# Kernel optimization log

Hardware: AMD Instinct MI355X
Metric: run time of the kernel (lower is better)

Reference implementation:

```python
import jax, jax.numpy as jnp
import numpy as np

TAU = 2.0
V_TH = 1.0
SG_ALPHA = 4.0  # spikingjelly surrogate.Sigmoid default

@jax.custom_vjp
def spike_fn(u):
    # heaviside(u) with sigmoid surrogate gradient; u = v - v_threshold
    return (u >= 0.0).astype(u.dtype)

def _spike_fwd(u):
    return spike_fn(u), u

def _spike_bwd(u, g):
    s = jax.nn.sigmoid(SG_ALPHA * u)
    return (g * SG_ALPHA * s * (1.0 - s),)

spike_fn.defvjp(_spike_fwd, _spike_bwd)

def lif_scan(h):
    # h: [T, B, D] input currents; multi-step LIF with hard reset to 0,
    # decay_input=True: v = v + (h - v) / tau
    def step(v, h_t):
        v = v + (h_t - v) / TAU
        s = spike_fn(v - V_TH)
        v = v * (1.0 - jax.lax.stop_gradient(s))  # detach_reset=True, v_reset=0
        return v, s
    v0 = jnp.zeros_like(h[0])
    _, spikes = jax.lax.scan(step, v0, h)
    return spikes  # [T, B, D]

def setup_inputs() -> dict:
    key = jax.random.key(0)
    k_x, k_w1, k_b1, k_w2, k_b2 = jax.random.split(key, 5)
    T, B, D, C = 32, 512, 1024, 1000
    lim1 = 1.0 / np.sqrt(D)
    return {
        "x": jax.random.normal(k_x, (T, B, D), dtype=jnp.float32),
        "W1": jax.random.uniform(k_w1, (D, D), jnp.float32, -lim1, lim1),
        "b1": jax.random.uniform(k_b1, (D,), jnp.float32, -lim1, lim1),
        "W2": jax.random.uniform(k_w2, (C, D), jnp.float32, -lim1, lim1),
        "b2": jax.random.uniform(k_b2, (C,), jnp.float32, -lim1, lim1),
    }

def reference(x, W1, b1, W2, b2):
    # linear_1: [T,B,D] @ [D,D]^T + b1
    h = jnp.einsum('tbd,ed->tbe', x, W1) + b1
    s = lif_scan(h)                               # [T,B,D] spikes in {0,1}
    y = jnp.einsum('tbd,cd->tbc', s, W2) + b2     # [T,B,C]
    y = y.mean(axis=0)                            # [B,C]
    return jax.nn.log_softmax(y, axis=1)
```

## Files before the change

### kernel.cpp

```cpp
#include <hip/hip_runtime.h>
#include <math.h>

#define T_STEPS 32
#define B_SZ    512
#define D_SZ    1024
#define C_SZ    1000
#define KZ      8
#define HP      132

typedef __bf16 bf16x8 __attribute__((ext_vector_type(8)));
typedef float  f32x4  __attribute__((ext_vector_type(4)));

__device__ __forceinline__ unsigned short f2bf(float f) {
    unsigned u = __float_as_uint(f);
    unsigned r = u + 0x7FFFu + ((u >> 16) & 1u);
    return (unsigned short)(r >> 16);
}
__device__ __forceinline__ float bf2f(unsigned short b) {
    return __uint_as_float(((unsigned)b) << 16);
}

__device__ __forceinline__ void async_copy16(const void* g, void* l) {
    __builtin_amdgcn_global_load_lds(
        (const __attribute__((address_space(1))) unsigned int*)g,
        (__attribute__((address_space(3))) unsigned int*)l,
        16, 0, 0);
}

__global__ __launch_bounds__(256) void cast_x_k(
    const float* __restrict__ s, unsigned short* __restrict__ d)
{
    const int idx = blockIdx.x * 256 + threadIdx.x;
    const float4 v = ((const float4*)s)[idx];
    ushort4 o;
    o.x = f2bf(v.x); o.y = f2bf(v.y); o.z = f2bf(v.z); o.w = f2bf(v.w);
    ((ushort4*)d)[idx] = o;
}

__global__ __launch_bounds__(256) void cast_w_k(
    const float* __restrict__ W1, unsigned short* __restrict__ W1o,
    const float* __restrict__ W2, unsigned short* __restrict__ W2o)
{
    const int idx = blockIdx.x * 256 + threadIdx.x;
    const int n1 = (D_SZ * D_SZ) / 4;
    const float4 v = (idx < n1) ? ((const float4*)W1)[idx]
                                : ((const float4*)W2)[idx - n1];
    ushort4 o;
    o.x = f2bf(v.x); o.y = f2bf(v.y); o.z = f2bf(v.z); o.w = f2bf(v.w);
    if (idx < n1) ((ushort4*)W1o)[idx] = o;
    else          ((ushort4*)W2o)[idx - n1] = o;
}

__global__ __launch_bounds__(256) void gemm1_scan_k(
    const unsigned short* __restrict__ A, const unsigned short* __restrict__ Bm,
    const float* __restrict__ bias, unsigned short* __restrict__ cnt)
{
    __shared__ __align__(16) unsigned short smem[128 * HP];
    unsigned short* As = smem;
    unsigned short* Bs = smem + 4096;

    const int tid  = threadIdx.x;
    const int wave = tid >> 6;
    const int lane = tid & 63;
    const int lm   = lane & 15;
    const int quad = lane >> 4;
    const int wm   = (wave >> 1) * 64;
    const int wn   = (wave & 1) * 64;

    const int f  = blockIdx.x;
    const int yb = f & 127;
    const int xb = f >> 7;
    const int b0 = yb * 4;
    const int n0 = xb * 128;

    f32x4 acc[4][4];
    #pragma unroll
    for (int i = 0; i < 4; ++i)
        #pragma unroll
        for (int j = 0; j < 4; ++j)
            acc[i][j] = (f32x4){0.f, 0.f, 0.f, 0.f};

    int srowA[2], sgq[2];
    size_t arowoff[2];
    unsigned ldsoff[2];
    #pragma unroll
    for (int p = 0; p < 2; ++p) {
        const int s = p * 256 + tid;
        const int rho = s >> 2;
        srowA[p] = rho;
        sgq[p]  = (s & 3) ^ ((rho >> 1) & 3);
        arowoff[p] = (size_t)((rho >> 2) * 512 + b0 + (rho & 3)) * D_SZ;
        ldsoff[p] = (unsigned)(p * 256 + wave * 64) * 16u;
    }
    const int fq = quad ^ ((lm >> 1) & 3);

    for (int k0 = 0; k0 < D_SZ; k0 += 32) {
        #pragma unroll
        for (int p = 0; p < 2; ++p) {
            async_copy16(A + arowoff[p] + k0 + sgq[p] * 8, (char*)As + ldsoff[p]);
            async_copy16(Bm + (size_t)(n0 + srowA[p]) * D_SZ + k0 + sgq[p] * 8,
                         (char*)Bs + ldsoff[p]);
        }
        __syncthreads();

        bf16x8 af[4], bfr[4];
        #pragma unroll
        for (int i = 0; i < 4; ++i) {
            af[i]  = ((const bf16x8*)As)[(wm + i * 16 + lm) * 4 + fq];
            bfr[i] = ((const bf16x8*)Bs)[(wn + i * 16 + lm) * 4 + fq];
        }
        #pragma unroll
        for (int mi = 0; mi < 4; ++mi)
            #pragma unroll
            for (int ni = 0; ni < 4; ++ni)
                acc[mi][ni] = __builtin_amdgcn_mfma_f32_16x16x32_bf16(
                    af[mi], bfr[ni], acc[mi][ni], 0, 0, 0);
        __syncthreads();
    }

    #pragma unroll
    for (int ni = 0; ni < 4; ++ni) {
        const int nn = wn + ni * 16 + lm;
        const float bv = bias[n0 + nn];
        #pragma unroll
        for (int mi = 0; mi < 4; ++mi) {
            const f32x4 v = acc[mi][ni];
            #pragma unroll
            for (int r = 0; r < 4; ++r)
                smem[(wm + mi * 16 + quad * 4 + r) * HP + nn] = f2bf(v[r] + bv);
        }
    }
    __syncthreads();

    #pragma unroll
    for (int rep = 0; rep < 2; ++rep) {
        const int flat = rep * 256 + tid;
        const int bb = flat >> 7;
        const int c  = flat & 127;
        float v = 0.f, cv = 0.f;
        #pragma unroll
        for (int t = 0; t < T_STEPS; ++t) {
            const float ht = bf2f(smem[(t * 4 + bb) * HP + c]);
            v = 0.5f * (v + ht);
            const float s = (v >= 1.0f) ? 1.0f : 0.0f;
            cv += s;
            v *= (1.0f - s);
        }
        cnt[(size_t)(b0 + bb) * D_SZ + n0 + c] = f2bf(cv);
    }
}

__global__ __launch_bounds__(256) void gemm2_splitk_k(
    const unsigned short* __restrict__ A, const unsigned short* __restrict__ Bm,
    float* __restrict__ partial)
{
    __shared__ __align__(16) unsigned short As[128 * 32];
    __shared__ __align__(16) unsigned short Bs[128 * 32];

    const int tid  = threadIdx.x;
    const int wave = tid >> 6;
    const int lane = tid & 63;
    const int lm   = lane & 15;
    const int quad = lane >> 4;
    const int wm   = (wave >> 1) * 64;
    const int wn   = (wave & 1) * 64;
    const int n0   = blockIdx.x * 128;
    const int m0   = blockIdx.y * 128;
    const int kz   = blockIdx.z;

    f32x4 acc[4][4];
    #pragma unroll
    for (int i = 0; i < 4; ++i)
        #pragma unroll
        for (int j = 0; j < 4; ++j)
            acc[i][j] = (f32x4){0.f, 0.f, 0.f, 0.f};

    int srow[2], sgq[2];
    unsigned ldsoff[2];
    #pragma unroll
    for (int p = 0; p < 2; ++p) {
        const int s = p * 256 + tid;
        srow[p] = s >> 2;
        sgq[p]  = (s & 3) ^ ((srow[p] >> 1) & 3);
        ldsoff[p] = (unsigned)(p * 256 + wave * 64) * 16u;
    }
    const int fq = quad ^ ((lm >> 1) & 3);

    const int kbeg = kz * (D_SZ / KZ);
    for (int k0 = kbeg; k0 < kbeg + D_SZ / KZ; k0 += 32) {
        #pragma unroll
        for (int p = 0; p < 2; ++p) {
            async_copy16(A + (size_t)(m0 + srow[p]) * D_SZ + k0 + sgq[p] * 8,
                         (char*)As + ldsoff[p]);
            int brow = n0 + srow[p];
            if (brow > C_SZ - 1) brow = C_SZ - 1;
            async_copy16(Bm + (size_t)brow * D_SZ + k0 + sgq[p] * 8,
                         (char*)Bs + ldsoff[p]);
        }
        __syncthreads();

        bf16x8 af[4], bfr[4];
        #pragma unroll
        for (int i = 0; i < 4; ++i) {
            af[i]  = ((const bf16x8*)As)[(wm + i * 16 + lm) * 4 + fq];
            bfr[i] = ((const bf16x8*)Bs)[(wn + i * 16 + lm) * 4 + fq];
        }
        #pragma unroll
        for (int mi = 0; mi < 4; ++mi)
            #pragma unroll
            for (int ni = 0; ni < 4; ++ni)
                acc[mi][ni] = __builtin_amdgcn_mfma_f32_16x16x32_bf16(
                    af[mi], bfr[ni], acc[mi][ni], 0, 0, 0);
        __syncthreads();
    }

    #pragma unroll
    for (int ni = 0; ni < 4; ++ni) {
        const int nn = n0 + wn + ni * 16 + lm;
        if (nn >= C_SZ) continue;
        #pragma unroll
        for (int mi = 0; mi < 4; ++mi) {
            const f32x4 v = acc[mi][ni];
            #pragma unroll
            for (int r = 0; r < 4; ++r) {
                const int mm = m0 + wm + mi * 16 + quad * 4 + r;
                partial[((size_t)kz * B_SZ + mm) * C_SZ + nn] = v[r];
            }
        }
    }
}

__global__ __launch_bounds__(256) void reduce_lsm_k(
    const float* __restrict__ partial, const float* __restrict__ b2,
    float* __restrict__ out)
{
    __shared__ float red_max[4];
    __shared__ float red_sum[4];

    const int b   = blockIdx.x;
    const int tid = threadIdx.x;

    float vals[4];
    float m = -1e30f;
    #pragma unroll
    for (int k = 0; k < 4; ++k) {
        const int c = tid + k * 256;
        if (c < C_SZ) {
            float s = 0.f;
            #pragma unroll
            for (int z = 0; z < KZ; ++z)
                s += partial[((size_t)z * B_SZ + b) * C_SZ + c];
            vals[k] = s * (1.0f / (float)T_STEPS) + b2[c];
        } else {
            vals[k] = -1e30f;
        }
        m = fmaxf(m, vals[k]);
    }
    #pragma unroll
    for (int off = 32; off > 0; off >>= 1)
        m = fmaxf(m, __shfl_down(m, off, 64));
    const int wave = tid >> 6;
    const int lane = tid & 63;
    if (lane == 0) red_max[wave] = m;
    __syncthreads();
    m = fmaxf(fmaxf(red_max[0], red_max[1]), fmaxf(red_max[2], red_max[3]));

    float s = 0.f;
    #pragma unroll
    for (int k = 0; k < 4; ++k) {
        const int c = tid + k * 256;
        if (c < C_SZ) s += __expf(vals[k] - m);
    }
    #pragma unroll
    for (int off = 32; off > 0; off >>= 1)
        s += __shfl_down(s, off, 64);
    if (lane == 0) red_sum[wave] = s;
    __syncthreads();
    s = red_sum[0] + red_sum[1] + red_sum[2] + red_sum[3];

    const float lse = m + logf(s);
    #pragma unroll
    for (int k = 0; k < 4; ++k) {
        const int c = tid + k * 256;
        if (c < C_SZ) out[(size_t)b * C_SZ + c] = vals[k] - lse;
    }
}

extern "C" void kernel_launch(void* const* d_in, const int* in_sizes, int n_in,
                              void* d_out, int out_size, void* d_ws, size_t ws_size,
                              hipStream_t stream)
{
    const float* x  = (const float*)d_in[0];
    const float* W1 = (const float*)d_in[1];
    const float* b1 = (const float*)d_in[2];
    const float* W2 = (const float*)d_in[3];
    const float* b2 = (const float*)d_in[4];
    float* out = (float*)d_out;

    char* ws = (char*)d_ws;
    unsigned short* x_bf    = (unsigned short*)(ws);
    unsigned short* W1_bf   = (unsigned short*)(ws + 33554432);
    unsigned short* W2_bf   = (unsigned short*)(ws + 35651584);
    unsigned short* cnt_bf  = (unsigned short*)(ws + 37699584);
    float*          partial = (float*)(ws + 38748160);

    const int MBD = T_STEPS * B_SZ;

    cast_x_k<<<(MBD * D_SZ / 4) / 256, 256, 0, stream>>>(x, x_bf);
    cast_w_k<<<((D_SZ * D_SZ + C_SZ * D_SZ) / 4) / 256, 256, 0, stream>>>(
        W1, W1_bf, W2, W2_bf);

    gemm1_scan_k<<<(B_SZ / 4) * (D_SZ / 128), 256, 0, stream>>>(
        x_bf, W1_bf, b1, cnt_bf);

    {
        dim3 grid((C_SZ + 127) / 128, B_SZ / 128, KZ);
        gemm2_splitk_k<<<grid, 256, 0, stream>>>(cnt_bf, W2_bf, partial);
    }

    reduce_lsm_k<<<B_SZ, 256, 0, stream>>>(partial, b2, out);
}
```

Before: 171.1 us.

## Fuse split-K reduction and log-softmax into GEMM2; merge cast and zeroing kernels

The two cast kernels become one that also zeroes the fp32 logits buffer and the per-row-block counters. GEMM2 now accumulates its split-K partials with float atomicAdd directly into y instead of writing a partial buffer. The last block to finish each 128-row group, found through an atomic counter, computes the mean, bias and log-softmax. This removes two launches and the partial buffer round trip. In exchange it adds atomic traffic, makes the float summation order nondeterministic, and leaves the softmax tail serialized on just four blocks.

```diff
diff --git a/kernel.cpp b/kernel.cpp
--- a/kernel.cpp
+++ b/kernel.cpp
@@ -27,28 +27,32 @@
         16, 0, 0);
 }
 
-__global__ __launch_bounds__(256) void cast_x_k(
-    const float* __restrict__ s, unsigned short* __restrict__ d)
+#define NX4  4194304
+#define NW14  262144
+#define NW24  256000
+#define NZ4   128001
+#define NTOT (NX4 + NW14 + NW24 + NZ4)
+
+__global__ __launch_bounds__(256) void cast_zero_k(
+    const float* __restrict__ x,  unsigned short* __restrict__ x_bf,
+    const float* __restrict__ W1, unsigned short* __restrict__ W1_bf,
+    const float* __restrict__ W2, unsigned short* __restrict__ W2_bf,
+    float4* __restrict__ zbase)
 {
     const int idx = blockIdx.x * 256 + threadIdx.x;
-    const float4 v = ((const float4*)s)[idx];
+    if (idx >= NTOT) return;
+    if (idx >= NX4 + NW14 + NW24) {
+        zbase[idx - (NX4 + NW14 + NW24)] = make_float4(0.f, 0.f, 0.f, 0.f);
+        return;
+    }
+    const float4* s; ushort4* d; int j;
+    if (idx < NX4)              { s = (const float4*)x;  d = (ushort4*)x_bf;  j = idx; }
+    else if (idx < NX4 + NW14)  { s = (const float4*)W1; d = (ushort4*)W1_bf; j = idx - NX4; }
+    else                        { s = (const float4*)W2; d = (ushort4*)W2_bf; j = idx - NX4 - NW14; }
+    const float4 v = s[j];
     ushort4 o;
     o.x = f2bf(v.x); o.y = f2bf(v.y); o.z = f2bf(v.z); o.w = f2bf(v.w);
-    ((ushort4*)d)[idx] = o;
-}
-
-__global__ __launch_bounds__(256) void cast_w_k(
-    const float* __restrict__ W1, unsigned short* __restrict__ W1o,
-    const float* __restrict__ W2, unsigned short* __restrict__ W2o)
-{
-    const int idx = blockIdx.x * 256 + threadIdx.x;
-    const int n1 = (D_SZ * D_SZ) / 4;
-    const float4 v = (idx < n1) ? ((const float4*)W1)[idx]
-                                : ((const float4*)W2)[idx - n1];
-    ushort4 o;
-    o.x = f2bf(v.x); o.y = f2bf(v.y); o.z = f2bf(v.z); o.w = f2bf(v.w);
-    if (idx < n1) ((ushort4*)W1o)[idx] = o;
-    else          ((ushort4*)W2o)[idx - n1] = o;
+    d[j] = o;
 }
 
 __global__ __launch_bounds__(256) void gemm1_scan_k(
@@ -150,12 +154,17 @@
     }
 }
 
-__global__ __launch_bounds__(256) void gemm2_splitk_k(
-    const unsigned short* __restrict__ A, const unsigned short* __restrict__ Bm,
-    float* __restrict__ partial)
+__global__ __launch_bounds__(256) void gemm2_lsm_k(
+    const unsigned short* __restrict__ A,
+    const unsigned short* __restrict__ Bm,
+    const float* __restrict__ b2,
+    float* __restrict__ y,
+    unsigned int* __restrict__ ctr,
+    float* __restrict__ out)
 {
     __shared__ __align__(16) unsigned short As[128 * 32];
     __shared__ __align__(16) unsigned short Bs[128 * 32];
+    __shared__ int lastFlag;
 
     const int tid  = threadIdx.x;
     const int wave = tid >> 6;
@@ -224,65 +233,63 @@
             #pragma unroll
             for (int r = 0; r < 4; ++r) {
                 const int mm = m0 + wm + mi * 16 + quad * 4 + r;
-                partial[((size_t)kz * B_SZ + mm) * C_SZ + nn] = v[r];
+                atomicAdd(&y[(size_t)mm * C_SZ + nn], v[r]);
             }
         }
     }
-}
-
-__global__ __launch_bounds__(256) void reduce_lsm_k(
-    const float* __restrict__ partial, const float* __restrict__ b2,
-    float* __restrict__ out)
-{
-    __shared__ float red_max[4];
-    __shared__ float red_sum[4];
-
-    const int b   = blockIdx.x;
-    const int tid = threadIdx.x;
-
-    float vals[4];
-    float m = -1e30f;
-    #pragma unroll
-    for (int k = 0; k < 4; ++k) {
-        const int c = tid + k * 256;
-        if (c < C_SZ) {
-            float s = 0.f;
-            #pragma unroll
-            for (int z = 0; z < KZ; ++z)
-                s += partial[((size_t)z * B_SZ + b) * C_SZ + c];
-            vals[k] = s * (1.0f / (float)T_STEPS) + b2[c];
-        } else {
-            vals[k] = -1e30f;
-        }
-        m = fmaxf(m, vals[k]);
-    }
-    #pragma unroll
-    for (int off = 32; off > 0; off >>= 1)
-        m = fmaxf(m, __shfl_down(m, off, 64));
-    const int wave = tid >> 6;
-    const int lane = tid & 63;
-    if (lane == 0) red_max[wave] = m;
+
+    __threadfence();
     __syncthreads();
-    m = fmaxf(fmaxf(red_max[0], red_max[1]), fmaxf(red_max[2], red_max[3]));
-
-    float s = 0.f;
-    #pragma unroll
-    for (int k = 0; k < 4; ++k) {
-        const int c = tid + k * 256;
-        if (c < C_SZ) s += __expf(vals[k] - m);
-    }
-    #pragma unroll
-    for (int off = 32; off > 0; off >>= 1)
-        s += __shfl_down(s, off, 64);
-    if (lane == 0) red_sum[wave] = s;
+    if (tid == 0) {
+        const unsigned old = atomicAdd(&ctr[blockIdx.y], 1u);
+        lastFlag = (old == (8 * KZ - 1)) ? 1 : 0;
+    }
     __syncthreads();
-    s = red_sum[0] + red_sum[1] + red_sum[2] + red_sum[3];
-
-    const float lse = m + logf(s);
-    #pragma unroll
-    for (int k = 0; k < 4; ++k) {
-        const int c = tid + k * 256;
-        if (c < C_SZ) out[(size_t)b * C_SZ + c] = vals[k] - lse;
+    if (!lastFlag) return;
+    __threadfence();
+
+    float* b2s = (float*)As;
+    for (int c = tid; c < C_SZ; c += 256) b2s[c] = b2[c];
+    __syncthreads();
+
+    const float inv = 1.0f / (float)T_STEPS;
+    for (int i = 0; i < 32; ++i) {
+        const int m = m0 + wave * 32 + i;
+        float vals[16];
+        float mx = -1e30f;
+        #pragma unroll
+        for (int s = 0; s < 16; ++s) {
+            const int c = s * 64 + lane;
+            float v = -1e30f;
+            if (c < C_SZ)
+                v = __hip_atomic_load(&y[(size_t)m * C_SZ + c],
+                                      __ATOMIC_RELAXED, __HIP_MEMORY_SCOPE_AGENT)
+                    * inv + b2s[c];
+            vals[s] = v;
+            mx = fmaxf(mx, v);
+        }
+        #pragma unroll
+        for (int off = 32; off > 0; off >>= 1)
+            mx = fmaxf(mx, __shfl_down(mx, off, 64));
+        mx = __shfl(mx, 0, 64);
+
+        float sm = 0.f;
+        #pragma unroll
+        for (int s = 0; s < 16; ++s) {
+            const int c = s * 64 + lane;
+            if (c < C_SZ) sm += __expf(vals[s] - mx);
+        }
+        #pragma unroll
+        for (int off = 32; off > 0; off >>= 1)
+            sm += __shfl_down(sm, off, 64);
+        sm = __shfl(sm, 0, 64);
+
+        const float lse = mx + logf(sm);
+        #pragma unroll
+        for (int s = 0; s < 16; ++s) {
+            const int c = s * 64 + lane;
+            if (c < C_SZ) out[(size_t)m * C_SZ + c] = vals[s] - lse;
+        }
     }
 }
 
@@ -298,25 +305,21 @@
     float* out = (float*)d_out;
 
     char* ws = (char*)d_ws;
-    unsigned short* x_bf    = (unsigned short*)(ws);
-    unsigned short* W1_bf   = (unsigned short*)(ws + 33554432);
-    unsigned short* W2_bf   = (unsigned short*)(ws + 35651584);
-    unsigned short* cnt_bf  = (unsigned short*)(ws + 37699584);
-    float*          partial = (float*)(ws + 38748160);
-
-    const int MBD = T_STEPS * B_SZ;
-
-    cast_x_k<<<(MBD * D_SZ / 4) / 256, 256, 0, stream>>>(x, x_bf);
-    cast_w_k<<<((D_SZ * D_SZ + C_SZ * D_SZ) / 4) / 256, 256, 0, stream>>>(
-        W1, W1_bf, W2, W2_bf);
+    unsigned short* x_bf   = (unsigned short*)(ws);
+    unsigned short* W1_bf  = (unsigned short*)(ws + 33554432);
+    unsigned short* W2_bf  = (unsigned short*)(ws + 35651584);
+    unsigned short* cnt_bf = (unsigned short*)(ws + 37699584);
+    float*          y32    = (float*)(ws + 38748160);
+    unsigned int*   ctr    = (unsigned int*)(ws + 40796160);
+
+    cast_zero_k<<<(NTOT + 255) / 256, 256, 0, stream>>>(
+        x, x_bf, W1, W1_bf, W2, W2_bf, (float4*)y32);
 
     gemm1_scan_k<<<(B_SZ / 4) * (D_SZ / 128), 256, 0, stream>>>(
         x_bf, W1_bf, b1, cnt_bf);
 
     {
         dim3 grid((C_SZ + 127) / 128, B_SZ / 128, KZ);
-        gemm2_splitk_k<<<grid, 256, 0, stream>>>(cnt_bf, W2_bf, partial);
-    }
-
-    reduce_lsm_k<<<B_SZ, 256, 0, stream>>>(partial, b2, out);
-}
+        gemm2_lsm_k<<<grid, 256, 0, stream>>>(cnt_bf, W2_bf, b2, y32, ctr, out);
+    }
+}
```

Result: slower. 230.1 us (+34.5%).

## Double GEMM1 K-tile to 64 and merge cast kernels into one launch

Applied to the files above, without the earlier changes.

The GEMM1+scan kernel now stages 64-wide K slices per iteration instead of 32, with an 8-way XOR swizzle in LDS and two MFMA sub-steps per barrier pair. This halves the number of synchronisation rounds and issues larger async copies per loop. Separately, the x and weight bf16 cast kernels are merged into one launch to save a kernel launch. The larger tile uses more LDS per stage, and the B buffer offset moves to 8192 to fit it.

```diff
diff --git a/kernel.cpp b/kernel.cpp
--- a/kernel.cpp
+++ b/kernel.cpp
@@ -27,28 +27,26 @@
         16, 0, 0);
 }
 
-__global__ __launch_bounds__(256) void cast_x_k(
-    const float* __restrict__ s, unsigned short* __restrict__ d)
+#define NX4  4194304
+#define NW14  262144
+#define NW24  256000
+#define NTOT (NX4 + NW14 + NW24)
+
+__global__ __launch_bounds__(256) void cast_k(
+    const float* __restrict__ x,  unsigned short* __restrict__ x_bf,
+    const float* __restrict__ W1, unsigned short* __restrict__ W1_bf,
+    const float* __restrict__ W2, unsigned short* __restrict__ W2_bf)
 {
     const int idx = blockIdx.x * 256 + threadIdx.x;
-    const float4 v = ((const float4*)s)[idx];
+    if (idx >= NTOT) return;
+    const float4* s; ushort4* d; int j;
+    if (idx < NX4)              { s = (const float4*)x;  d = (ushort4*)x_bf;  j = idx; }
+    else if (idx < NX4 + NW14)  { s = (const float4*)W1; d = (ushort4*)W1_bf; j = idx - NX4; }
+    else                        { s = (const float4*)W2; d = (ushort4*)W2_bf; j = idx - NX4 - NW14; }
+    const float4 v = s[j];
     ushort4 o;
     o.x = f2bf(v.x); o.y = f2bf(v.y); o.z = f2bf(v.z); o.w = f2bf(v.w);
-    ((ushort4*)d)[idx] = o;
-}
-
-__global__ __launch_bounds__(256) void cast_w_k(
-    const float* __restrict__ W1, unsigned short* __restrict__ W1o,
-    const float* __restrict__ W2, unsigned short* __restrict__ W2o)
-{
-    const int idx = blockIdx.x * 256 + threadIdx.x;
-    const int n1 = (D_SZ * D_SZ) / 4;
-    const float4 v = (idx < n1) ? ((const float4*)W1)[idx]
-                                : ((const float4*)W2)[idx - n1];
-    ushort4 o;
-    o.x = f2bf(v.x); o.y = f2bf(v.y); o.z = f2bf(v.z); o.w = f2bf(v.w);
-    if (idx < n1) ((ushort4*)W1o)[idx] = o;
-    else          ((ushort4*)W2o)[idx - n1] = o;
+    d[j] = o;
 }
 
 __global__ __launch_bounds__(256) void gemm1_scan_k(
@@ -57,7 +55,7 @@
 {
     __shared__ __align__(16) unsigned short smem[128 * HP];
     unsigned short* As = smem;
-    unsigned short* Bs = smem + 4096;
+    unsigned short* Bs = smem + 8192;
 
     const int tid  = threadIdx.x;
     const int wave = tid >> 6;
@@ -80,41 +78,45 @@
         for (int j = 0; j < 4; ++j)
             acc[i][j] = (f32x4){0.f, 0.f, 0.f, 0.f};
 
-    int srowA[2], sgq[2];
-    size_t arowoff[2];
-    unsigned ldsoff[2];
-    #pragma unroll
-    for (int p = 0; p < 2; ++p) {
+    int srow[4], sgq[4];
+    size_t arowoff[4];
+    unsigned ldsoff[4];
+    #pragma unroll
+    for (int p = 0; p < 4; ++p) {
         const int s = p * 256 + tid;
-        const int rho = s >> 2;
-        srowA[p] = rho;
-        sgq[p]  = (s & 3) ^ ((rho >> 1) & 3);
+        const int rho = s >> 3;
+        srow[p] = rho;
+        sgq[p]  = (s & 7) ^ (rho & 7);
         arowoff[p] = (size_t)((rho >> 2) * 512 + b0 + (rho & 3)) * D_SZ;
         ldsoff[p] = (unsigned)(p * 256 + wave * 64) * 16u;
     }
-    const int fq = quad ^ ((lm >> 1) & 3);
-
-    for (int k0 = 0; k0 < D_SZ; k0 += 32) {
-        #pragma unroll
-        for (int p = 0; p < 2; ++p) {
+    const int fq0 = quad ^ (lm & 7);
+
+    for (int k0 = 0; k0 < D_SZ; k0 += 64) {
+        #pragma unroll
+        for (int p = 0; p < 4; ++p) {
             async_copy16(A + arowoff[p] + k0 + sgq[p] * 8, (char*)As + ldsoff[p]);
-            async_copy16(Bm + (size_t)(n0 + srowA[p]) * D_SZ + k0 + sgq[p] * 8,
+            async_copy16(Bm + (size_t)(n0 + srow[p]) * D_SZ + k0 + sgq[p] * 8,
                          (char*)Bs + ldsoff[p]);
         }
         __syncthreads();
 
-        bf16x8 af[4], bfr[4];
-        #pragma unroll
-        for (int i = 0; i < 4; ++i) {
-            af[i]  = ((const bf16x8*)As)[(wm + i * 16 + lm) * 4 + fq];
-            bfr[i] = ((const bf16x8*)Bs)[(wn + i * 16 + lm) * 4 + fq];
-        }
-        #pragma unroll
-        for (int mi = 0; mi < 4; ++mi)
-            #pragma unroll
-            for (int ni = 0; ni < 4; ++ni)
-                acc[mi][ni] = __builtin_amdgcn_mfma_f32_16x16x32_bf16(
-                    af[mi], bfr[ni], acc[mi][ni], 0, 0, 0);
+        #pragma unroll
+        for (int kk = 0; kk < 2; ++kk) {
+            const int fqk = fq0 ^ (kk * 4);
+            bf16x8 af[4], bfr[4];
+            #pragma unroll
+            for (int i = 0; i < 4; ++i) {
+                af[i]  = ((const bf16x8*)As)[(wm + i * 16 + lm) * 8 + fqk];
+                bfr[i] = ((const bf16x8*)Bs)[(wn + i * 16 + lm) * 8 + fqk];
+            }
+            #pragma unroll
+            for (int mi = 0; mi < 4; ++mi)
+                #pragma unroll
+                for (int ni = 0; ni < 4; ++ni)
+                    acc[mi][ni] = __builtin_amdgcn_mfma_f32_16x16x32_bf16(
+                        af[mi], bfr[ni], acc[mi][ni], 0, 0, 0);
+        }
         __syncthreads();
     }
 
@@ -304,11 +306,8 @@
     unsigned short* cnt_bf  = (unsigned short*)(ws + 37699584);
     float*          partial = (float*)(ws + 38748160);
 
-    const int MBD = T_STEPS * B_SZ;
-
-    cast_x_k<<<(MBD * D_SZ / 4) / 256, 256, 0, stream>>>(x, x_bf);
-    cast_w_k<<<((D_SZ * D_SZ + C_SZ * D_SZ) / 4) / 256, 256, 0, stream>>>(
-        W1, W1_bf, W2, W2_bf);
+    cast_k<<<(NTOT + 255) / 256, 256, 0, stream>>>(
+        x, x_bf, W1, W1_bf, W2, W2_bf);
 
     gemm1_scan_k<<<(B_SZ / 4) * (D_SZ / 128), 256, 0, stream>>>(
         x_bf, W1_bf, b1, cnt_bf);
```

Measured after the change: 164.5 us. 3.9% less time.
